# Kernel tuning notes

Hardware: AMD Instinct MI355X
Metric: run time of the kernel (lower is better)

## Reference

```python
import jax, jax.numpy as jnp
import numpy as np

EPS_COS = 1e-16   # epsilon added to operands (as in the torch module)
EPS_NRM = 1e-8    # torch cosine_similarity clamps norms at 1e-8


def setup_inputs() -> dict:
    key = jax.random.key(0)
    k0, k1, k2, k3, k4, k5 = jax.random.split(key, 6)
    B, N, M = 64, 2048, 256
    stdev = 1.0 / np.sqrt(N + M)
    memory = jax.random.uniform(k0, (B, N, M), jnp.float32, -stdev, stdev)
    k = jax.random.normal(k1, (B, M), jnp.float32)
    g = jax.random.uniform(k2, (B, 1), jnp.float32)
    gamma = jax.random.uniform(k3, (1,), jnp.float32)
    # w_prev[:,0] = w_u_prev, w_prev[:,1] = w_r_prev (positive weightings)
    w_prev = jax.random.uniform(k4, (B, 2, N), jnp.float32)
    # w_lu_prev is a 0/1 least-recently-used mask
    w_lu_prev = jax.random.randint(k5, (B, N), 0, 2, jnp.int32)
    return {"memory": memory, "k": k, "g": g, "gamma": gamma,
            "w_prev": w_prev, "w_lu_prev": w_lu_prev, "n": 4}


def reference(memory, k, g, gamma, w_prev, w_lu_prev, n):
    # --- _similarity: softmax over cosine similarity along memory slots ---
    mem_e = memory + EPS_COS                      # [B, N, M]
    k_e = k[:, None, :] + EPS_COS                 # [B, 1, M]
    num = jnp.einsum('bnm,bom->bn', mem_e, k_e)   # [B, N]
    mem_nrm = jnp.maximum(jnp.linalg.norm(mem_e, axis=-1), EPS_NRM)
    k_nrm = jnp.maximum(jnp.linalg.norm(k_e, axis=-1), EPS_NRM)  # [B, 1]
    w_r = jax.nn.softmax(num / (mem_nrm * k_nrm), axis=-1)       # [B, N]

    # --- interpolate write weighting and usage weighting ---
    w_u_prev = w_prev[:, 0]                        # [B, N]
    w_r_prev = w_prev[:, 1]                        # [B, N]
    w_lu_prev_f = w_lu_prev.astype(memory.dtype)   # [B, N], 0/1 mask
    w_w = g * w_r_prev + (1.0 - g) * w_lu_prev_f   # [B, N]
    w_u = gamma * w_u_prev + w_r + w_w             # [B, N]

    # --- least-used mask: w_u <= n-th smallest usage (per batch) ---
    nth_smallest = jnp.sort(w_u, axis=1)[:, n - 1]           # [B]
    w_lu = (w_u <= nth_smallest[:, None]).astype(memory.dtype)  # [B, N]

    # --- zero out slots that were least-recently-used last step ---
    mem_zeroed = memory * (1.0 - w_lu_prev_f)[..., None]      # [B, N, M]

    # --- lrua_write: rank-1 outer-product write, then read with w_r ---
    mem_new = mem_zeroed + w_w[..., None] * k[:, None, :]     # [B, N, M]
    read = jnp.einsum('bn,bnm->bm', w_r, mem_new)             # [B, M]
    return read
```

## Files before the change

kernel.cpp:

```cpp
#include <hip/hip_runtime.h>
#include <math.h>

#define EPS_COS 1e-16f
#define EPS_NRM 1e-8f

constexpr int B = 64;
constexpr int N = 2048;
constexpr int M = 256;

constexpr int BLK    = 256;
constexpr int WAVES  = BLK / 64;
constexpr int CHUNK  = 64;
constexpr int RPW    = CHUNK / WAVES;
constexpr int NCHUNK = N / CHUNK;

__global__ __launch_bounds__(BLK)
void k1_fused(const float* __restrict__ mem,
              const float* __restrict__ kk,
              const float* __restrict__ g,
              const float* __restrict__ w_prev,
              const int*   __restrict__ lu_prev,
              float* __restrict__ pread,
              float* __restrict__ pZ,
              float* __restrict__ pS1)
{
    const int b    = blockIdx.y;
    const int c    = blockIdx.x;
    const int tid  = threadIdx.x;
    const int w    = tid >> 6;
    const int lane = tid & 63;

    float4 kv = *reinterpret_cast<const float4*>(kk + (size_t)b * M + lane * 4);
    kv.x += EPS_COS; kv.y += EPS_COS; kv.z += EPS_COS; kv.w += EPS_COS;
    float ksq = kv.x*kv.x + kv.y*kv.y + kv.z*kv.z + kv.w*kv.w;
#pragma unroll
    for (int off = 32; off; off >>= 1) ksq += __shfl_xor(ksq, off);
    const float kn = fmaxf(sqrtf(ksq), EPS_NRM);

    const float gb   = g[b];
    const float* wrp = w_prev + (size_t)b * 2 * N + N;
    const int*   lup = lu_prev + (size_t)b * N;

    const int rowbase = c * CHUNK + w * RPW;
    const float* p = mem + ((size_t)b * N + rowbase) * M + lane * 4;

    float4 acc = make_float4(0.f, 0.f, 0.f, 0.f);
    float Zp = 0.f, s1p = 0.f;

    auto process = [&](int i, const float4& v) {
        float m0 = v.x + EPS_COS, m1 = v.y + EPS_COS;
        float m2 = v.z + EPS_COS, m3 = v.w + EPS_COS;
        float dot = m0*kv.x + m1*kv.y + m2*kv.z + m3*kv.w;
        float msq = m0*m0 + m1*m1 + m2*m2 + m3*m3;
#pragma unroll
        for (int off = 32; off; off >>= 1) {
            dot += __shfl_xor(dot, off);
            msq += __shfl_xor(msq, off);
        }
        const int n = rowbase + i;
        const float cosv = dot / (fmaxf(sqrtf(msq), EPS_NRM) * kn);
        const float e  = __expf(cosv);
        const float lu = (float)lup[n];
        const float ww = gb * wrp[n] + (1.f - gb) * lu;
        Zp += e;
        s1p = fmaf(e, ww, s1p);
        const float cw = e * (1.f - lu);
        acc.x = fmaf(cw, v.x, acc.x);
        acc.y = fmaf(cw, v.y, acc.y);
        acc.z = fmaf(cw, v.z, acc.z);
        acc.w = fmaf(cw, v.w, acc.w);
    };

    float4 v0 = *reinterpret_cast<const float4*>(p);
    float4 v1 = *reinterpret_cast<const float4*>(p + (size_t)1 * M);
    float4 v2 = *reinterpret_cast<const float4*>(p + (size_t)2 * M);
    float4 v3 = *reinterpret_cast<const float4*>(p + (size_t)3 * M);
#pragma unroll
    for (int i = 0; i < RPW - 4; ++i) {
        float4 v4 = *reinterpret_cast<const float4*>(p + (size_t)(i + 4) * M);
        process(i, v0);
        v0 = v1; v1 = v2; v2 = v3; v3 = v4;
    }
    process(RPW - 4, v0);
    process(RPW - 3, v1);
    process(RPW - 2, v2);
    process(RPW - 1, v3);

    __shared__ float sred[WAVES * M];
    __shared__ float sZ[WAVES], sS1[WAVES];
    *reinterpret_cast<float4*>(&sred[w * M + lane * 4]) = acc;
    if (lane == 0) { sZ[w] = Zp; sS1[w] = s1p; }
    __syncthreads();

    {
        float r = 0.f;
#pragma unroll
        for (int q = 0; q < WAVES; ++q) r += sred[q * M + tid];
        pread[((size_t)b * NCHUNK + c) * M + tid] = r;
    }
    if (tid == 0) {
        float z = 0.f, s = 0.f;
#pragma unroll
        for (int q = 0; q < WAVES; ++q) { z += sZ[q]; s += sS1[q]; }
        pZ[b * NCHUNK + c]  = z;
        pS1[b * NCHUNK + c] = s;
    }
}

__global__ __launch_bounds__(M)
void k2_final(const float* __restrict__ pread,
              const float* __restrict__ pZ,
              const float* __restrict__ pS1,
              const float* __restrict__ kk,
              float* __restrict__ out)
{
    const int b = blockIdx.x;
    const int t = threadIdx.x;
    float z = 0.f, s = 0.f;
#pragma unroll
    for (int q = 0; q < NCHUNK; ++q) {
        z += pZ[b * NCHUNK + q];
        s += pS1[b * NCHUNK + q];
    }
    const float* pr = pread + (size_t)b * NCHUNK * M + t;
    float sum = 0.f;
#pragma unroll
    for (int q = 0; q < NCHUNK; ++q) sum += pr[(size_t)q * M];
    out[(size_t)b * M + t] = (sum + s * kk[(size_t)b * M + t]) / z;
}

extern "C" void kernel_launch(void* const* d_in, const int* in_sizes, int n_in,
                              void* d_out, int out_size, void* d_ws, size_t ws_size,
                              hipStream_t stream) {
    const float* mem     = (const float*)d_in[0];
    const float* kk      = (const float*)d_in[1];
    const float* g       = (const float*)d_in[2];
    const float* w_prev  = (const float*)d_in[4];
    const int*   lu_prev = (const int*)  d_in[5];
    float* out = (float*)d_out;

    float* pread = (float*)d_ws;
    float* pZ    = pread + (size_t)B * NCHUNK * M;
    float* pS1   = pZ + (size_t)B * NCHUNK;

    dim3 g1(NCHUNK, B);
    k1_fused<<<g1, BLK, 0, stream>>>(mem, kk, g, w_prev, lu_prev, pread, pZ, pS1);
    k2_final<<<B, M, 0, stream>>>(pread, pZ, pS1, kk, out);
}
```

Before: 34.16 us.

## Remap lanes so each wave reduces eight rows with short shuffles

The thread mapping changes so that each group of 8 lanes covers one memory row, and a wave handles 8 rows at a time. This cuts the per-row cross-lane reduction from a 6-step, 64-wide shuffle to 3 shuffle steps shared across 8 rows. Each lane now keeps 8 float4 accumulators, and the shared-memory reduction is padded to avoid bank conflicts. CHUNK doubles, which halves the number of blocks. The 1e-16 epsilon additions are dropped because they do not change fp32 results at these magnitudes, and the Z/S1 sums are scaled by 1/8 to undo the replication across the 8 lanes. Register pressure rises because of the 8-wide accumulator and load arrays.

```diff
diff --git a/kernel.cpp b/kernel.cpp
--- a/kernel.cpp
+++ b/kernel.cpp
@@ -1,7 +1,6 @@
 #include <hip/hip_runtime.h>
 #include <math.h>
 
-#define EPS_COS 1e-16f
 #define EPS_NRM 1e-8f
 
 constexpr int B = 64;
@@ -10,9 +9,11 @@
 
 constexpr int BLK    = 256;
 constexpr int WAVES  = BLK / 64;
-constexpr int CHUNK  = 64;
+constexpr int CHUNK  = 128;
 constexpr int RPW    = CHUNK / WAVES;
+constexpr int G      = RPW / 8;
 constexpr int NCHUNK = N / CHUNK;
+constexpr int LROW   = M + 4;
 
 __global__ __launch_bounds__(BLK)
 void k1_fused(const float* __restrict__ mem,
@@ -29,12 +30,21 @@
     const int tid  = threadIdx.x;
     const int w    = tid >> 6;
     const int lane = tid & 63;
+    const int rg   = lane >> 3;
+    const int l8   = lane & 7;
 
-    float4 kv = *reinterpret_cast<const float4*>(kk + (size_t)b * M + lane * 4);
-    kv.x += EPS_COS; kv.y += EPS_COS; kv.z += EPS_COS; kv.w += EPS_COS;
-    float ksq = kv.x*kv.x + kv.y*kv.y + kv.z*kv.z + kv.w*kv.w;
+    float4 kf[8];
+    const float* kp = kk + (size_t)b * M;
 #pragma unroll
-    for (int off = 32; off; off >>= 1) ksq += __shfl_xor(ksq, off);
+    for (int j = 0; j < 8; ++j)
+        kf[j] = *reinterpret_cast<const float4*>(kp + l8 * 4 + j * 32);
+    float ksq = 0.f;
+#pragma unroll
+    for (int j = 0; j < 8; ++j)
+        ksq += kf[j].x*kf[j].x + kf[j].y*kf[j].y + kf[j].z*kf[j].z + kf[j].w*kf[j].w;
+    ksq += __shfl_xor(ksq, 1);
+    ksq += __shfl_xor(ksq, 2);
+    ksq += __shfl_xor(ksq, 4);
     const float kn = fmaxf(sqrtf(ksq), EPS_NRM);
 
     const float gb   = g[b];
@@ -42,22 +52,38 @@
     const int*   lup = lu_prev + (size_t)b * N;
 
     const int rowbase = c * CHUNK + w * RPW;
-    const float* p = mem + ((size_t)b * N + rowbase) * M + lane * 4;
+    const float* pbase = mem + ((size_t)b * N + rowbase + rg) * M + l8 * 4;
 
-    float4 acc = make_float4(0.f, 0.f, 0.f, 0.f);
+    float4 acc[8];
+#pragma unroll
+    for (int j = 0; j < 8; ++j) acc[j] = make_float4(0.f, 0.f, 0.f, 0.f);
     float Zp = 0.f, s1p = 0.f;
 
-    auto process = [&](int i, const float4& v) {
-        float m0 = v.x + EPS_COS, m1 = v.y + EPS_COS;
-        float m2 = v.z + EPS_COS, m3 = v.w + EPS_COS;
-        float dot = m0*kv.x + m1*kv.y + m2*kv.z + m3*kv.w;
-        float msq = m0*m0 + m1*m1 + m2*m2 + m3*m3;
 #pragma unroll
-        for (int off = 32; off; off >>= 1) {
-            dot += __shfl_xor(dot, off);
-            msq += __shfl_xor(msq, off);
+    for (int gi = 0; gi < G; ++gi) {
+        const float* p = pbase + (size_t)gi * 8 * M;
+        float4 v[8];
+#pragma unroll
+        for (int j = 0; j < 8; ++j)
+            v[j] = *reinterpret_cast<const float4*>(p + j * 32);
+
+        float dot = 0.f, msq = 0.f;
+#pragma unroll
+        for (int j = 0; j < 8; ++j) {
+            dot = fmaf(v[j].x, kf[j].x, dot);
+            dot = fmaf(v[j].y, kf[j].y, dot);
+            dot = fmaf(v[j].z, kf[j].z, dot);
+            dot = fmaf(v[j].w, kf[j].w, dot);
+            msq = fmaf(v[j].x, v[j].x, msq);
+            msq = fmaf(v[j].y, v[j].y, msq);
+            msq = fmaf(v[j].z, v[j].z, msq);
+            msq = fmaf(v[j].w, v[j].w, msq);
         }
-        const int n = rowbase + i;
+        dot += __shfl_xor(dot, 1);  msq += __shfl_xor(msq, 1);
+        dot += __shfl_xor(dot, 2);  msq += __shfl_xor(msq, 2);
+        dot += __shfl_xor(dot, 4);  msq += __shfl_xor(msq, 4);
+
+        const int n = rowbase + gi * 8 + rg;
         const float cosv = dot / (fmaxf(sqrtf(msq), EPS_NRM) * kn);
         const float e  = __expf(cosv);
         const float lu = (float)lup[n];
@@ -65,37 +91,34 @@
         Zp += e;
         s1p = fmaf(e, ww, s1p);
         const float cw = e * (1.f - lu);
-        acc.x = fmaf(cw, v.x, acc.x);
-        acc.y = fmaf(cw, v.y, acc.y);
-        acc.z = fmaf(cw, v.z, acc.z);
-        acc.w = fmaf(cw, v.w, acc.w);
-    };
+#pragma unroll
+        for (int j = 0; j < 8; ++j) {
+            acc[j].x = fmaf(cw, v[j].x, acc[j].x);
+            acc[j].y = fmaf(cw, v[j].y, acc[j].y);
+            acc[j].z = fmaf(cw, v[j].z, acc[j].z);
+            acc[j].w = fmaf(cw, v[j].w, acc[j].w);
+        }
+    }
 
-    float4 v0 = *reinterpret_cast<const float4*>(p);
-    float4 v1 = *reinterpret_cast<const float4*>(p + (size_t)1 * M);
-    float4 v2 = *reinterpret_cast<const float4*>(p + (size_t)2 * M);
-    float4 v3 = *reinterpret_cast<const float4*>(p + (size_t)3 * M);
 #pragma unroll
-    for (int i = 0; i < RPW - 4; ++i) {
-        float4 v4 = *reinterpret_cast<const float4*>(p + (size_t)(i + 4) * M);
-        process(i, v0);
-        v0 = v1; v1 = v2; v2 = v3; v3 = v4;
+    for (int off = 32; off; off >>= 1) {
+        Zp  += __shfl_xor(Zp, off);
+        s1p += __shfl_xor(s1p, off);
     }
-    process(RPW - 4, v0);
-    process(RPW - 3, v1);
-    process(RPW - 2, v2);
-    process(RPW - 1, v3);
 
-    __shared__ float sred[WAVES * M];
+    __shared__ float sacc[WAVES * 8 * LROW];
     __shared__ float sZ[WAVES], sS1[WAVES];
-    *reinterpret_cast<float4*>(&sred[w * M + lane * 4]) = acc;
-    if (lane == 0) { sZ[w] = Zp; sS1[w] = s1p; }
+    float* dst = &sacc[(w * 8 + rg) * LROW + l8 * 4];
+#pragma unroll
+    for (int j = 0; j < 8; ++j)
+        *reinterpret_cast<float4*>(dst + j * 32) = acc[j];
+    if (lane == 0) { sZ[w] = Zp * 0.125f; sS1[w] = s1p * 0.125f; }
     __syncthreads();
 
     {
         float r = 0.f;
 #pragma unroll
-        for (int q = 0; q < WAVES; ++q) r += sred[q * M + tid];
+        for (int q = 0; q < WAVES * 8; ++q) r += sacc[q * LROW + tid];
         pread[((size_t)b * NCHUNK + c) * M + tid] = r;
     }
     if (tid == 0) {
```

Measured after the change: 30.52 us. 10.7% less time.
